# Optimization experiments

Hardware: AMD Instinct MI355X
Metric: run time of the kernel (lower is better)

Reference implementation:

```python
import jax, jax.numpy as jnp
import numpy as np

LN_EPS = 1e-5


def setup_inputs() -> dict:
    key = jax.random.key(0)
    ks = jax.random.split(key, 6)
    N, E, D = 100000, 600000, 128
    x = jax.random.normal(ks[0], (N, D), dtype=jnp.float32)
    edge_index = jax.random.randint(ks[1], (2, E), 0, N, dtype=jnp.int64)
    dropout_mask = jax.random.uniform(ks[2], (N, D), dtype=jnp.float32)
    ln_gamma = jnp.ones((D,), dtype=jnp.float32)
    ln_beta = jnp.zeros((D,), dtype=jnp.float32)
    W_l = jax.random.normal(ks[3], (D, D), dtype=jnp.float32) / np.sqrt(D)
    b_l = jnp.zeros((D,), dtype=jnp.float32)
    W_r = jax.random.normal(ks[4], (D, D), dtype=jnp.float32) / np.sqrt(D)
    return {"x": x, "edge_index": edge_index, "dropout_mask": dropout_mask,
            "ln_gamma": ln_gamma, "ln_beta": ln_beta,
            "W_l": W_l, "b_l": b_l, "W_r": W_r}


def reference(x, edge_index, dropout_mask, ln_gamma, ln_beta, W_l, b_l, W_r):
    N = x.shape[0]
    # LayerNorm (elementwise affine) -> ReLU -> dropout mask
    mu = jnp.mean(x, axis=-1, keepdims=True)
    var = jnp.mean(jnp.square(x - mu), axis=-1, keepdims=True)
    h = (x - mu) * jax.lax.rsqrt(var + LN_EPS) * ln_gamma + ln_beta
    h = jax.nn.relu(h) * dropout_mask  # [N, D]
    # SAGEConv with mean aggregation: messages flow src -> dst
    src, dst = edge_index[0], edge_index[1]
    agg = jax.ops.segment_sum(h[src], dst, num_segments=N)  # [N, D]
    cnt = jax.ops.segment_sum(jnp.ones_like(dst, dtype=h.dtype), dst,
                              num_segments=N)
    mean_agg = agg / jnp.maximum(cnt, 1.0)[:, None]
    # out = lin_l(mean_agg) + lin_r(h); PyG stores weights as [out, in]
    return mean_agg @ W_l.T + b_l + h @ W_r.T
```

## Files before the change

kernel.cpp:

```cpp
#include <hip/hip_runtime.h>

#define LN_EPS 1e-5f
#define D 128
#define SCAN_CHUNK 1024
#define LDSA_STRIDE 264
#define NBF 128

typedef __attribute__((ext_vector_type(4))) float f32x4;
typedef __attribute__((ext_vector_type(8))) short bf16x8;

static __device__ __forceinline__ ushort f2bf(float f) {
    union { float f; unsigned u; } a; a.f = f;
    unsigned r = a.u + 0x7FFF + ((a.u >> 16) & 1);
    return (ushort)(r >> 16);
}
static __device__ __forceinline__ float bf2f(ushort u) {
    union { unsigned u; float f; } a; a.u = ((unsigned)u) << 16;
    return a.f;
}

static __device__ __forceinline__ void gbar(int* ctr, int target) {
    __syncthreads();
    if (threadIdx.x == 0) {
        __hip_atomic_fetch_add(ctr, 1, __ATOMIC_ACQ_REL, __HIP_MEMORY_SCOPE_AGENT);
        while (__hip_atomic_load(ctr, __ATOMIC_ACQUIRE,
                                 __HIP_MEMORY_SCOPE_AGENT) < target)
            __builtin_amdgcn_s_sleep(8);
    }
    __syncthreads();
}

__global__ void mega(const float* __restrict__ x, const int* __restrict__ ei,
                     const float* __restrict__ mask,
                     const float* __restrict__ gamma,
                     const float* __restrict__ beta,
                     const float* __restrict__ Wl,
                     const float* __restrict__ Wr,
                     ushort* __restrict__ hbf, ushort* __restrict__ Bfrag,
                     int* __restrict__ hist, int* __restrict__ offs,
                     int* __restrict__ cursor, int* __restrict__ csums,
                     int* __restrict__ bar, int* __restrict__ ssrc,
                     int N, int E, int nph) {
    __shared__ int slds[256];
    __shared__ int base_s;
    const int bid = (int)blockIdx.x;
    const int tid = (int)threadIdx.x;

    if (bid >= nph + NBF) {
        int lane = tid & 63;
        int wid  = (bid - nph - NBF) * 4 + (tid >> 6);
        int g2   = lane >> 4;
        int sl   = lane & 15;
        int node = wid * 4 + g2;
        if (node >= N) return;

        const float* xr = x + (size_t)node * D + sl * 8;
        f32x4 v0 = *(const f32x4*)xr;
        f32x4 v1 = *(const f32x4*)(xr + 4);
        const float* mr = mask + (size_t)node * D + sl * 8;
        f32x4 m0 = *(const f32x4*)mr;
        f32x4 m1 = *(const f32x4*)(mr + 4);

        float s  = (v0.x + v0.y) + (v0.z + v0.w) + (v1.x + v1.y) + (v1.z + v1.w);
        float ss = (v0.x * v0.x + v0.y * v0.y) + (v0.z * v0.z + v0.w * v0.w)
                 + (v1.x * v1.x + v1.y * v1.y) + (v1.z * v1.z + v1.w * v1.w);
#pragma unroll
        for (int off = 8; off > 0; off >>= 1) {
            s  += __shfl_xor(s, off);
            ss += __shfl_xor(ss, off);
        }
        float mu  = s * (1.0f / D);
        float var = ss * (1.0f / D) - mu * mu;
        float rs  = rsqrtf(var + LN_EPS);

        f32x4 g0 = *(const f32x4*)(gamma + sl * 8);
        f32x4 g1 = *(const f32x4*)(gamma + sl * 8 + 4);
        f32x4 b0 = *(const f32x4*)(beta + sl * 8);
        f32x4 b1 = *(const f32x4*)(beta + sl * 8 + 4);

        bf16x8 o;
        o[0] = (short)f2bf(fmaxf((v0.x - mu) * rs * g0.x + b0.x, 0.0f) * m0.x);
        o[1] = (short)f2bf(fmaxf((v0.y - mu) * rs * g0.y + b0.y, 0.0f) * m0.y);
        o[2] = (short)f2bf(fmaxf((v0.z - mu) * rs * g0.z + b0.z, 0.0f) * m0.z);
        o[3] = (short)f2bf(fmaxf((v0.w - mu) * rs * g0.w + b0.w, 0.0f) * m0.w);
        o[4] = (short)f2bf(fmaxf((v1.x - mu) * rs * g1.x + b1.x, 0.0f) * m1.x);
        o[5] = (short)f2bf(fmaxf((v1.y - mu) * rs * g1.y + b1.y, 0.0f) * m1.y);
        o[6] = (short)f2bf(fmaxf((v1.z - mu) * rs * g1.z + b1.z, 0.0f) * m1.z);
        o[7] = (short)f2bf(fmaxf((v1.w - mu) * rs * g1.w + b1.w, 0.0f) * m1.w);
        *(bf16x8*)(hbf + (size_t)node * D + sl * 8) = o;
        return;
    }

    if (bid >= nph) {
        int t = (bid - nph) * 256 + tid;
        int i    = t & 7;
        int lane = (t >> 3) & 63;
        int jb   = (t >> 9) & 7;
        int ks   = t >> 12;
        int k = ks * 32 + (lane >> 4) * 8 + i;
        int j = jb * 16 + (lane & 15);
        float v = (k < D) ? Wl[j * D + k] : Wr[j * D + (k - D)];
        Bfrag[t] = f2bf(v);
        return;
    }

    const int pt  = bid * 256 + tid;
    const int PTN = nph * 256;
    const int* dst = ei + E;
    const int nq = E >> 2;

    for (int c = pt; c < nq; c += PTN) {
        int4 d = *(const int4*)(dst + c * 4);
        atomicAdd(&hist[d.x], 1);
        atomicAdd(&hist[d.y], 1);
        atomicAdd(&hist[d.z], 1);
        atomicAdd(&hist[d.w], 1);
    }
    for (int e = (nq << 2) + pt; e < E; e += PTN) atomicAdd(&hist[dst[e]], 1);
    gbar(&bar[0], nph);

    {
        int base = bid * SCAN_CHUNK;
        int idx0 = base + tid * 4;
        int v[4];
#pragma unroll
        for (int i = 0; i < 4; i++) {
            int idx = idx0 + i;
            v[i] = (idx < N) ? __hip_atomic_load(&hist[idx], __ATOMIC_RELAXED,
                                                 __HIP_MEMORY_SCOPE_AGENT) : 0;
        }
        slds[tid] = v[0] + v[1] + v[2] + v[3];
        __syncthreads();
        for (int off = 1; off < 256; off <<= 1) {
            int add = (tid >= off) ? slds[tid - off] : 0;
            __syncthreads();
            slds[tid] += add;
            __syncthreads();
        }
        int run = (tid == 0) ? 0 : slds[tid - 1];
        if (tid == 255)
            __hip_atomic_store(&csums[bid], slds[255] | 0x40000000,
                               __ATOMIC_RELEASE, __HIP_MEMORY_SCOPE_AGENT);
        if (tid < 64) {
            int acc = 0;
            for (int c = tid; c < bid; c += 64) {
                int w;
                do {
                    w = __hip_atomic_load(&csums[c], __ATOMIC_ACQUIRE,
                                          __HIP_MEMORY_SCOPE_AGENT);
                } while (!(w & 0x40000000));
                acc += w & 0x3FFFFFFF;
            }
#pragma unroll
            for (int off = 32; off > 0; off >>= 1) acc += __shfl_xor(acc, off);
            if (tid == 0) base_s = acc;
        }
        __syncthreads();
        run += base_s;
#pragma unroll
        for (int i = 0; i < 4; i++) {
            int idx = idx0 + i;
            if (idx < N) {
                __hip_atomic_store(&offs[idx], run, __ATOMIC_RELAXED,
                                   __HIP_MEMORY_SCOPE_AGENT);
                __hip_atomic_store(&cursor[idx], run, __ATOMIC_RELAXED,
                                   __HIP_MEMORY_SCOPE_AGENT);
            }
            run += v[i];
        }
    }
    gbar(&bar[1], nph);

    for (int c = pt; c < nq; c += PTN) {
        int4 d = *(const int4*)(dst + c * 4);
        int4 s = *(const int4*)(ei + c * 4);
        int p0 = atomicAdd(&cursor[d.x], 1);
        int p1 = atomicAdd(&cursor[d.y], 1);
        int p2 = atomicAdd(&cursor[d.z], 1);
        int p3 = atomicAdd(&cursor[d.w], 1);
        ssrc[p0] = s.x;
        ssrc[p1] = s.y;
        ssrc[p2] = s.z;
        ssrc[p3] = s.w;
    }
    for (int e = (nq << 2) + pt; e < E; e += PTN) {
        int pos = atomicAdd(&cursor[dst[e]], 1);
        ssrc[pos] = ei[e];
    }
}

__global__ void __launch_bounds__(256, 4)
agg_gemm(float* __restrict__ out,
         const ushort* __restrict__ hbf,
         const int* __restrict__ sorted_src,
         const int* __restrict__ offs,
         const int* __restrict__ hist,
         const ushort* __restrict__ Bfrag,
         const float* __restrict__ bl,
         int N, int E) {
    __shared__ ushort Alds[64 * LDSA_STRIDE];
    int tid  = threadIdx.x;
    int wave = tid >> 6;
    int lane = tid & 63;
    int n0 = blockIdx.x * 64;

#pragma unroll
    for (int it = 0; it < 4; it++) {
        int chunk = tid + 256 * it;
        int row = chunk >> 4;
        int c8  = chunk & 15;
        int node = n0 + row;
        bf16x8 vh = (bf16x8){0,0,0,0,0,0,0,0};
        if (node < N) vh = *(const bf16x8*)(hbf + (size_t)node * D + c8 * 8);
        *(bf16x8*)&Alds[row * LDSA_STRIDE + 128 + c8 * 8] = vh;
    }

    int g  = lane >> 4;
    int sl = lane & 15;
    int row0 = wave * 16 + g;
    int start[4], deg[4], dm1[4];
#pragma unroll
    for (int p = 0; p < 4; p++) {
        int node = n0 + row0 + p * 4;
        start[p] = 0; deg[p] = 0;
        if (node < N) { start[p] = offs[node]; deg[p] = hist[node]; }
        dm1[p] = deg[p] - 1; if (dm1[p] < 0) dm1[p] = 0;
    }
    float acc[4][8];
#pragma unroll
    for (int p = 0; p < 4; p++)
#pragma unroll
        for (int q = 0; q < 8; q++) acc[p][q] = 0.0f;

    int dmax = max(max(deg[0], deg[1]), max(deg[2], deg[3]));
    int Em = E - 1;
    int ia[4], ib[4];
#pragma unroll
    for (int p = 0; p < 4; p++) {
        int pa = start[p];                         if (pa > Em) pa = Em;
        int j1 = (1 < dm1[p]) ? 1 : dm1[p];
        int pb = start[p] + j1;                    if (pb > Em) pb = Em;
        ia[p] = sorted_src[pa];
        ib[p] = sorted_src[pb];
    }
    for (int j = 0; j < dmax; j += 2) {
        int ca[4], cb[4];
#pragma unroll
        for (int p = 0; p < 4; p++) { ca[p] = ia[p]; cb[p] = ib[p]; }
#pragma unroll
        for (int p = 0; p < 4; p++) {
            int j2 = (j + 2 < dm1[p]) ? j + 2 : dm1[p];
            int j3 = (j + 3 < dm1[p]) ? j + 3 : dm1[p];
            int pa = start[p] + j2; if (pa > Em) pa = Em;
            int pb = start[p] + j3; if (pb > Em) pb = Em;
            ia[p] = sorted_src[pa];
            ib[p] = sorted_src[pb];
        }
#pragma unroll
        for (int p = 0; p < 4; p++) {
            bf16x8 v = *(const bf16x8*)(hbf + (size_t)ca[p] * D + sl * 8);
            float m = (j < deg[p]) ? 1.0f : 0.0f;
#pragma unroll
            for (int q = 0; q < 8; q++) acc[p][q] += bf2f((ushort)v[q]) * m;
        }
#pragma unroll
        for (int p = 0; p < 4; p++) {
            bf16x8 v = *(const bf16x8*)(hbf + (size_t)cb[p] * D + sl * 8);
            float m = (j + 1 < deg[p]) ? 1.0f : 0.0f;
#pragma unroll
            for (int q = 0; q < 8; q++) acc[p][q] += bf2f((ushort)v[q]) * m;
        }
    }
#pragma unroll
    for (int p = 0; p < 4; p++) {
        float inv = 1.0f / fmaxf((float)deg[p], 1.0f);
        bf16x8 o;
#pragma unroll
        for (int q = 0; q < 8; q++) o[q] = (short)f2bf(acc[p][q] * inv);
        *(bf16x8*)&Alds[(row0 + p * 4) * LDSA_STRIDE + sl * 8] = o;
    }
    __syncthreads();

    bf16x8 breg[8][2];
#pragma unroll
    for (int ks = 0; ks < 8; ks++)
#pragma unroll
        for (int jj = 0; jj < 2; jj++) {
            int jb = wave * 2 + jj;
            breg[ks][jj] = *(const bf16x8*)(Bfrag + (size_t)((ks * 8 + jb) * 64 + lane) * 8);
        }

    f32x4 acc2[4][2];
#pragma unroll
    for (int nb = 0; nb < 4; nb++)
#pragma unroll
        for (int jj = 0; jj < 2; jj++)
            acc2[nb][jj] = (f32x4){0.f, 0.f, 0.f, 0.f};

    int arow = lane & 15;
    int akoff = (lane >> 4) * 8;
#pragma unroll
    for (int ks = 0; ks < 8; ks++) {
#pragma unroll
        for (int nb = 0; nb < 4; nb++) {
            bf16x8 a = *(const bf16x8*)&Alds[(nb * 16 + arow) * LDSA_STRIDE + ks * 32 + akoff];
            acc2[nb][0] = __builtin_amdgcn_mfma_f32_16x16x32_bf16(a, breg[ks][0], acc2[nb][0], 0, 0, 0);
            acc2[nb][1] = __builtin_amdgcn_mfma_f32_16x16x32_bf16(a, breg[ks][1], acc2[nb][1], 0, 0, 0);
        }
    }

    float bias0 = bl[wave * 32 + (lane & 15)];
    float bias1 = bl[wave * 32 + 16 + (lane & 15)];
    int rbase = (lane >> 4) * 4;
#pragma unroll
    for (int nb = 0; nb < 4; nb++) {
#pragma unroll
        for (int r = 0; r < 4; r++) {
            int row = nb * 16 + rbase + r;
            if (n0 + row < N) {
                float* orow = out + (size_t)(n0 + row) * D + wave * 32 + (lane & 15);
                orow[0]  = acc2[nb][0][r] + bias0;
                orow[16] = acc2[nb][1][r] + bias1;
            }
        }
    }
}

extern "C" void kernel_launch(void* const* d_in, const int* in_sizes, int n_in,
                              void* d_out, int out_size, void* d_ws, size_t ws_size,
                              hipStream_t stream) {
    const float* x     = (const float*)d_in[0];
    const int*   ei    = (const int*)  d_in[1];
    const float* mask  = (const float*)d_in[2];
    const float* gamma = (const float*)d_in[3];
    const float* beta  = (const float*)d_in[4];
    const float* Wl    = (const float*)d_in[5];
    const float* bl    = (const float*)d_in[6];
    const float* Wr    = (const float*)d_in[7];
    float* out = (float*)d_out;

    int N = in_sizes[0] / D;
    int E = in_sizes[1] / 2;
    int nph = (N + SCAN_CHUNK - 1) / SCAN_CHUNK;

    ushort* hbf   = (ushort*)d_ws;
    ushort* Bfrag = hbf + (size_t)N * D;
    int* hist   = (int*)(Bfrag + 32768);
    int* csums  = hist + N;
    int* bar    = csums + 128;
    int* offs   = bar + 16;
    int* cursor = offs + N;
    int* ssrc   = cursor + N;

    int lnBlocks = (N + 15) / 16;

    hipMemsetAsync(hist, 0, (size_t)(N + 144) * sizeof(int), stream);
    mega<<<nph + NBF + lnBlocks, 256, 0, stream>>>(x, ei, mask, gamma, beta,
                                                   Wl, Wr, hbf, Bfrag, hist,
                                                   offs, cursor, csums, bar,
                                                   ssrc, N, E, nph);
    agg_gemm<<<(N + 63) / 64, 256, 0, stream>>>(out, hbf, ssrc, offs, hist,
                                                Bfrag, bl, N, E);
}
```

Measured before the change: 257.9 us.

## Run all mega-kernel phases on a persistent 1024-block grid

Result: slower. 413.1 us (+60.1%).

```diff
diff --git a/kernel.cpp b/kernel.cpp
--- a/kernel.cpp
+++ b/kernel.cpp
@@ -4,7 +4,7 @@
 #define D 128
 #define SCAN_CHUNK 1024
 #define LDSA_STRIDE 264
-#define NBF 128
+#define GRID 1024
 
 typedef __attribute__((ext_vector_type(4))) float f32x4;
 typedef __attribute__((ext_vector_type(8))) short bf16x8;
@@ -40,138 +40,94 @@
                      int* __restrict__ hist, int* __restrict__ offs,
                      int* __restrict__ cursor, int* __restrict__ csums,
                      int* __restrict__ bar, int* __restrict__ ssrc,
-                     int N, int E, int nph) {
+                     int N, int E) {
     __shared__ int slds[256];
     __shared__ int base_s;
     const int bid = (int)blockIdx.x;
     const int tid = (int)threadIdx.x;
-
-    if (bid >= nph + NBF) {
-        int lane = tid & 63;
-        int wid  = (bid - nph - NBF) * 4 + (tid >> 6);
-        int g2   = lane >> 4;
-        int sl   = lane & 15;
-        int node = wid * 4 + g2;
-        if (node >= N) return;
-
-        const float* xr = x + (size_t)node * D + sl * 8;
-        f32x4 v0 = *(const f32x4*)xr;
-        f32x4 v1 = *(const f32x4*)(xr + 4);
-        const float* mr = mask + (size_t)node * D + sl * 8;
-        f32x4 m0 = *(const f32x4*)mr;
-        f32x4 m1 = *(const f32x4*)(mr + 4);
-
-        float s  = (v0.x + v0.y) + (v0.z + v0.w) + (v1.x + v1.y) + (v1.z + v1.w);
-        float ss = (v0.x * v0.x + v0.y * v0.y) + (v0.z * v0.z + v0.w * v0.w)
-                 + (v1.x * v1.x + v1.y * v1.y) + (v1.z * v1.z + v1.w * v1.w);
-#pragma unroll
-        for (int off = 8; off > 0; off >>= 1) {
-            s  += __shfl_xor(s, off);
-            ss += __shfl_xor(ss, off);
-        }
-        float mu  = s * (1.0f / D);
-        float var = ss * (1.0f / D) - mu * mu;
-        float rs  = rsqrtf(var + LN_EPS);
-
-        f32x4 g0 = *(const f32x4*)(gamma + sl * 8);
-        f32x4 g1 = *(const f32x4*)(gamma + sl * 8 + 4);
-        f32x4 b0 = *(const f32x4*)(beta + sl * 8);
-        f32x4 b1 = *(const f32x4*)(beta + sl * 8 + 4);
-
-        bf16x8 o;
-        o[0] = (short)f2bf(fmaxf((v0.x - mu) * rs * g0.x + b0.x, 0.0f) * m0.x);
-        o[1] = (short)f2bf(fmaxf((v0.y - mu) * rs * g0.y + b0.y, 0.0f) * m0.y);
-        o[2] = (short)f2bf(fmaxf((v0.z - mu) * rs * g0.z + b0.z, 0.0f) * m0.z);
-        o[3] = (short)f2bf(fmaxf((v0.w - mu) * rs * g0.w + b0.w, 0.0f) * m0.w);
-        o[4] = (short)f2bf(fmaxf((v1.x - mu) * rs * g1.x + b1.x, 0.0f) * m1.x);
-        o[5] = (short)f2bf(fmaxf((v1.y - mu) * rs * g1.y + b1.y, 0.0f) * m1.y);
-        o[6] = (short)f2bf(fmaxf((v1.z - mu) * rs * g1.z + b1.z, 0.0f) * m1.z);
-        o[7] = (short)f2bf(fmaxf((v1.w - mu) * rs * g1.w + b1.w, 0.0f) * m1.w);
-        *(bf16x8*)(hbf + (size_t)node * D + sl * 8) = o;
-        return;
-    }
-
-    if (bid >= nph) {
-        int t = (bid - nph) * 256 + tid;
-        int i    = t & 7;
-        int lane = (t >> 3) & 63;
-        int jb   = (t >> 9) & 7;
-        int ks   = t >> 12;
+    const int gt  = bid * 256 + tid;
+    const int GT  = GRID * 256;
+    const int target = (int)gridDim.x;
+
+    if (gt < 8 * 8 * 64 * 8) {
+        int i    = gt & 7;
+        int lane = (gt >> 3) & 63;
+        int jb   = (gt >> 9) & 7;
+        int ks   = gt >> 12;
         int k = ks * 32 + (lane >> 4) * 8 + i;
         int j = jb * 16 + (lane & 15);
         float v = (k < D) ? Wl[j * D + k] : Wr[j * D + (k - D)];
-        Bfrag[t] = f2bf(v);
-        return;
-    }
-
-    const int pt  = bid * 256 + tid;
-    const int PTN = nph * 256;
+        Bfrag[gt] = f2bf(v);
+    }
+
     const int* dst = ei + E;
     const int nq = E >> 2;
-
-    for (int c = pt; c < nq; c += PTN) {
+    for (int c = gt; c < nq; c += GT) {
         int4 d = *(const int4*)(dst + c * 4);
         atomicAdd(&hist[d.x], 1);
         atomicAdd(&hist[d.y], 1);
         atomicAdd(&hist[d.z], 1);
         atomicAdd(&hist[d.w], 1);
     }
-    for (int e = (nq << 2) + pt; e < E; e += PTN) atomicAdd(&hist[dst[e]], 1);
-    gbar(&bar[0], nph);
+    for (int e = (nq << 2) + gt; e < E; e += GT) atomicAdd(&hist[dst[e]], 1);
+    gbar(&bar[0], target);
 
     {
-        int base = bid * SCAN_CHUNK;
-        int idx0 = base + tid * 4;
-        int v[4];
-#pragma unroll
-        for (int i = 0; i < 4; i++) {
-            int idx = idx0 + i;
-            v[i] = (idx < N) ? __hip_atomic_load(&hist[idx], __ATOMIC_RELAXED,
-                                                 __HIP_MEMORY_SCOPE_AGENT) : 0;
-        }
-        slds[tid] = v[0] + v[1] + v[2] + v[3];
-        __syncthreads();
-        for (int off = 1; off < 256; off <<= 1) {
-            int add = (tid >= off) ? slds[tid - off] : 0;
+        int nchunks = (N + SCAN_CHUNK - 1) / SCAN_CHUNK;
+        if (bid < nchunks) {
+            int base = bid * SCAN_CHUNK;
+            int idx0 = base + tid * 4;
+            int v[4];
+#pragma unroll
+            for (int i = 0; i < 4; i++) {
+                int idx = idx0 + i;
+                v[i] = (idx < N) ? __hip_atomic_load(&hist[idx], __ATOMIC_RELAXED,
+                                                     __HIP_MEMORY_SCOPE_AGENT) : 0;
+            }
+            slds[tid] = v[0] + v[1] + v[2] + v[3];
             __syncthreads();
-            slds[tid] += add;
+            for (int off = 1; off < 256; off <<= 1) {
+                int add = (tid >= off) ? slds[tid - off] : 0;
+                __syncthreads();
+                slds[tid] += add;
+                __syncthreads();
+            }
+            int run = (tid == 0) ? 0 : slds[tid - 1];
+            if (tid == 255)
+                __hip_atomic_store(&csums[bid], slds[255] | 0x40000000,
+                                   __ATOMIC_RELEASE, __HIP_MEMORY_SCOPE_AGENT);
+            if (tid < 64) {
+                int acc = 0;
+                for (int c = tid; c < bid; c += 64) {
+                    int w;
+                    do {
+                        w = __hip_atomic_load(&csums[c], __ATOMIC_ACQUIRE,
+                                              __HIP_MEMORY_SCOPE_AGENT);
+                    } while (!(w & 0x40000000));
+                    acc += w & 0x3FFFFFFF;
+                }
+#pragma unroll
+                for (int off = 32; off > 0; off >>= 1) acc += __shfl_xor(acc, off);
+                if (tid == 0) base_s = acc;
+            }
             __syncthreads();
-        }
-        int run = (tid == 0) ? 0 : slds[tid - 1];
-        if (tid == 255)
-            __hip_atomic_store(&csums[bid], slds[255] | 0x40000000,
-                               __ATOMIC_RELEASE, __HIP_MEMORY_SCOPE_AGENT);
-        if (tid < 64) {
-            int acc = 0;
-            for (int c = tid; c < bid; c += 64) {
-                int w;
-                do {
-                    w = __hip_atomic_load(&csums[c], __ATOMIC_ACQUIRE,
-                                          __HIP_MEMORY_SCOPE_AGENT);
-                } while (!(w & 0x40000000));
-                acc += w & 0x3FFFFFFF;
-            }
-#pragma unroll
-            for (int off = 32; off > 0; off >>= 1) acc += __shfl_xor(acc, off);
-            if (tid == 0) base_s = acc;
-        }
-        __syncthreads();
-        run += base_s;
-#pragma unroll
-        for (int i = 0; i < 4; i++) {
-            int idx = idx0 + i;
-            if (idx < N) {
-                __hip_atomic_store(&offs[idx], run, __ATOMIC_RELAXED,
-                                   __HIP_MEMORY_SCOPE_AGENT);
-                __hip_atomic_store(&cursor[idx], run, __ATOMIC_RELAXED,
-                                   __HIP_MEMORY_SCOPE_AGENT);
-            }
-            run += v[i];
-        }
-    }
-    gbar(&bar[1], nph);
-
-    for (int c = pt; c < nq; c += PTN) {
+            run += base_s;
+#pragma unroll
+            for (int i = 0; i < 4; i++) {
+                int idx = idx0 + i;
+                if (idx < N) {
+                    __hip_atomic_store(&offs[idx], run, __ATOMIC_RELAXED,
+                                       __HIP_MEMORY_SCOPE_AGENT);
+                    __hip_atomic_store(&cursor[idx], run, __ATOMIC_RELAXED,
+                                       __HIP_MEMORY_SCOPE_AGENT);
+                }
+                run += v[i];
+            }
+        }
+    }
+    gbar(&bar[1], target);
+
+    for (int c = gt; c < nq; c += GT) {
         int4 d = *(const int4*)(dst + c * 4);
         int4 s = *(const int4*)(ei + c * 4);
         int p0 = atomicAdd(&cursor[d.x], 1);
@@ -183,9 +139,55 @@
         ssrc[p2] = s.z;
         ssrc[p3] = s.w;
     }
-    for (int e = (nq << 2) + pt; e < E; e += PTN) {
+    for (int e = (nq << 2) + gt; e < E; e += GT) {
         int pos = atomicAdd(&cursor[dst[e]], 1);
         ssrc[pos] = ei[e];
+    }
+
+    {
+        int w  = gt >> 6;
+        int nw = GT >> 6;
+        int lane = tid & 63;
+        int g2 = (lane >> 4);
+        int sl = lane & 15;
+        for (int np = w; np * 4 < N; np += nw) {
+            int node = np * 4 + g2;
+            if (node >= N) continue;
+            const float* xr = x + (size_t)node * D + sl * 8;
+            f32x4 v0 = *(const f32x4*)xr;
+            f32x4 v1 = *(const f32x4*)(xr + 4);
+            const float* mr = mask + (size_t)node * D + sl * 8;
+            f32x4 m0 = *(const f32x4*)mr;
+            f32x4 m1 = *(const f32x4*)(mr + 4);
+
+            float s  = (v0.x + v0.y) + (v0.z + v0.w) + (v1.x + v1.y) + (v1.z + v1.w);
+            float ss = (v0.x * v0.x + v0.y * v0.y) + (v0.z * v0.z + v0.w * v0.w)
+                     + (v1.x * v1.x + v1.y * v1.y) + (v1.z * v1.z + v1.w * v1.w);
+#pragma unroll
+            for (int off = 8; off > 0; off >>= 1) {
+                s  += __shfl_xor(s, off);
+                ss += __shfl_xor(ss, off);
+            }
+            float mu  = s * (1.0f / D);
+            float var = ss * (1.0f / D) - mu * mu;
+            float rs  = rsqrtf(var + LN_EPS);
+
+            f32x4 g0 = *(const f32x4*)(gamma + sl * 8);
+            f32x4 g1 = *(const f32x4*)(gamma + sl * 8 + 4);
+            f32x4 b0 = *(const f32x4*)(beta + sl * 8);
+            f32x4 b1 = *(const f32x4*)(beta + sl * 8 + 4);
+
+            bf16x8 o;
+            o[0] = (short)f2bf(fmaxf((v0.x - mu) * rs * g0.x + b0.x, 0.0f) * m0.x);
+            o[1] = (short)f2bf(fmaxf((v0.y - mu) * rs * g0.y + b0.y, 0.0f) * m0.y);
+            o[2] = (short)f2bf(fmaxf((v0.z - mu) * rs * g0.z + b0.z, 0.0f) * m0.z);
+            o[3] = (short)f2bf(fmaxf((v0.w - mu) * rs * g0.w + b0.w, 0.0f) * m0.w);
+            o[4] = (short)f2bf(fmaxf((v1.x - mu) * rs * g1.x + b1.x, 0.0f) * m1.x);
+            o[5] = (short)f2bf(fmaxf((v1.y - mu) * rs * g1.y + b1.y, 0.0f) * m1.y);
+            o[6] = (short)f2bf(fmaxf((v1.z - mu) * rs * g1.z + b1.z, 0.0f) * m1.z);
+            o[7] = (short)f2bf(fmaxf((v1.w - mu) * rs * g1.w + b1.w, 0.0f) * m1.w);
+            *(bf16x8*)(hbf + (size_t)node * D + sl * 8) = o;
+        }
     }
 }
 
@@ -341,7 +343,6 @@
 
     int N = in_sizes[0] / D;
     int E = in_sizes[1] / 2;
-    int nph = (N + SCAN_CHUNK - 1) / SCAN_CHUNK;
 
     ushort* hbf   = (ushort*)d_ws;
     ushort* Bfrag = hbf + (size_t)N * D;
@@ -352,13 +353,10 @@
     int* cursor = offs + N;
     int* ssrc   = cursor + N;
 
-    int lnBlocks = (N + 15) / 16;
-
     hipMemsetAsync(hist, 0, (size_t)(N + 144) * sizeof(int), stream);
-    mega<<<nph + NBF + lnBlocks, 256, 0, stream>>>(x, ei, mask, gamma, beta,
-                                                   Wl, Wr, hbf, Bfrag, hist,
-                                                   offs, cursor, csums, bar,
-                                                   ssrc, N, E, nph);
+    mega<<<GRID, 256, 0, stream>>>(x, ei, mask, gamma, beta, Wl, Wr,
+                                   hbf, Bfrag, hist, offs, cursor, csums,
+                                   bar, ssrc, N, E);
     agg_gemm<<<(N + 63) / 64, 256, 0, stream>>>(out, hbf, ssrc, offs, hist,
                                                 Bfrag, bl, N, E);
 }
```
